# Performance work log

Hardware: AMD Instinct MI355X
Metric: run time of the kernel (lower is better)

## Reference

```python
import jax, jax.numpy as jnp
import numpy as np

C_CLAMP = 0.5
EPSILON = 1e-6
L_START = 0

BATCH, SEQ, D_MODEL, N_EXPERTS, RANK = 4, 8192, 1024, 16, 16


def setup_inputs() -> dict:
    key = jax.random.key(0)
    k_x, k_w, k_a, k_b, k_s = jax.random.split(key, 5)
    x = jax.random.normal(k_x, (BATCH, SEQ, D_MODEL), dtype=jnp.float32)
    # base nn.Linear params
    W = jax.random.normal(k_w, (D_MODEL, D_MODEL), dtype=jnp.float32) * 0.02
    b = jnp.zeros((D_MODEL,), dtype=jnp.float32)
    # stacked per-expert LoRA factors: A_e [in, r], B_e [r, out]
    A = jax.random.normal(k_a, (N_EXPERTS, D_MODEL, RANK), dtype=jnp.float32) * 0.02
    B_mat = jax.random.normal(k_b, (N_EXPERTS, RANK, D_MODEL), dtype=jnp.float32) * 0.02
    # routing scores p_score per active expert
    scores = jax.random.uniform(k_s, (N_EXPERTS,), dtype=jnp.float32)
    layer_idx = 5  # static python int, >= L_START so adapters are injected
    return {"x": x, "W": W, "b": b, "A": A, "B_mat": B_mat,
            "scores": scores, "layer_idx": layer_idx}


def reference(x, W, b, A, B_mat, scores, layer_idx):
    # base linear: z = x @ W^T + b
    z = jnp.einsum('bsd,Dd->bsD', x, W) + b
    if layer_idx is not None and layer_idx < L_START:
        return z
    # m = sum_e p_e * (x @ A_e @ B_e), batched low-rank adapter sum
    xa = jnp.einsum('bsd,edr->ebsr', x, A)          # [E, B, S, r]
    m = jnp.einsum('e,ebsr,erD->bsD', scores, xa, B_mat)
    # norm-ratio clamp epilogue
    norm_z = jnp.linalg.norm(z, axis=-1, keepdims=True)
    norm_m = jnp.linalg.norm(m, axis=-1, keepdims=True)
    gamma = jnp.minimum(C_CLAMP * norm_z / (norm_m + EPSILON), 1.0)
    return z + gamma * m
```

## Files before the change

kernel.cpp:

```cpp
#include <hip/hip_runtime.h>

typedef __attribute__((ext_vector_type(8))) __bf16 bf16x8;
typedef __attribute__((ext_vector_type(8))) unsigned short u16x8;
typedef __attribute__((ext_vector_type(4))) float f32x4;

__device__ inline unsigned short f2bf(float f) {
    union { float f; unsigned int i; } v; v.f = f;
    unsigned int i = v.i;
    unsigned int r = i + 0x7FFFu + ((i >> 16) & 1u);
    return (unsigned short)(r >> 16);
}
__device__ inline float bf2f(unsigned short u) {
    union { unsigned int i; float f; } v; v.i = ((unsigned int)u) << 16; return v.f;
}

__device__ inline void gload_lds16(const void* g, void* l) {
    __builtin_amdgcn_global_load_lds(
        (const __attribute__((address_space(1))) unsigned int*)g,
        (__attribute__((address_space(3))) unsigned int*)l, 16, 0, 0);
}

__device__ inline bf16x8 ldsrd(unsigned off) {
    bf16x8 r;
    asm volatile("ds_read_b128 %0, %1" : "=v"(r) : "v"(off));
    return r;
}

__global__ __launch_bounds__(256) void cast_x(const float* __restrict__ x,
                                              unsigned short* __restrict__ xb, int n4) {
    int idx = blockIdx.x * blockDim.x + threadIdx.x;
    int stride = gridDim.x * blockDim.x;
    for (int i = idx; i < n4; i += stride) {
        float4 v = ((const float4*)x)[i];
        ushort4 o;
        o.x = f2bf(v.x); o.y = f2bf(v.y); o.z = f2bf(v.z); o.w = f2bf(v.w);
        ((ushort4*)xb)[i] = o;
    }
}

__global__ __launch_bounds__(256) void cast_w(const float* __restrict__ W,
                                              unsigned short* __restrict__ wcat) {
    int i = blockIdx.x * 256 + threadIdx.x;
    float4 v = ((const float4*)W)[i];
    ushort4 o;
    o.x = f2bf(v.x); o.y = f2bf(v.y); o.z = f2bf(v.z); o.w = f2bf(v.w);
    ((ushort4*)wcat)[i] = o;
}

__global__ __launch_bounds__(256) void prep_acat(const float* __restrict__ A,
                                                 const float* __restrict__ scores,
                                                 unsigned short* __restrict__ acat) {
    int tid = blockIdx.x * 256 + threadIdx.x;
    int e = tid >> 10;
    int d = tid & 1023;
    float pe = scores[e];
    const float4* src = (const float4*)(A + (size_t)e * 16384 + (size_t)d * 16);
    unsigned short* dst = acat + (size_t)d * 256 + e * 16;
    #pragma unroll
    for (int q = 0; q < 4; ++q) {
        float4 v = src[q];
        ushort4 o;
        o.x = f2bf(pe * v.x); o.y = f2bf(pe * v.y);
        o.z = f2bf(pe * v.z); o.w = f2bf(pe * v.w);
        *(ushort4*)(dst + q * 4) = o;
    }
}

__global__ __launch_bounds__(256) void prep_bcat(const float* __restrict__ Bm,
                                                 unsigned short* __restrict__ bcatT) {
    __shared__ float t[64][65];
    const int tx = threadIdx.x;
    const int Dt = (blockIdx.x & 15) * 64;
    const int et = (blockIdx.x >> 4) * 64;
    {
        const int i = tx >> 2;
        const int c4 = (tx & 3) * 16;
        const float* src = Bm + (size_t)(et + i) * 1024 + Dt + c4;
        #pragma unroll
        for (int q = 0; q < 4; ++q) {
            float4 v = *(const float4*)(src + q * 4);
            t[i][c4 + q * 4 + 0] = v.x; t[i][c4 + q * 4 + 1] = v.y;
            t[i][c4 + q * 4 + 2] = v.z; t[i][c4 + q * 4 + 3] = v.w;
        }
    }
    __syncthreads();
    {
        const int j = tx >> 2;
        const int seg = (tx & 3) * 16;
        unsigned short* dst = bcatT + (size_t)(Dt + j) * 256 + et + seg;
        #pragma unroll
        for (int q = 0; q < 16; ++q)
            dst[q] = f2bf(t[seg + q][j]);
    }
}

__global__ __launch_bounds__(256) void mini_gemm(const unsigned short* __restrict__ bcatT,
                                                 const unsigned short* __restrict__ acat,
                                                 unsigned short* __restrict__ wcat) {
    extern __shared__ char lds[];
    const int tid = threadIdx.x;
    const int l = tid & 63;
    const int w = tid >> 6;
    const int wr = w >> 1;
    const int wc = w & 1;

    const int trow = (blockIdx.x >> 3) * 128;
    const int tcol = (blockIdx.x & 7) * 128;

    const unsigned rA128 = (unsigned)((wr * 64 + (l & 15)) * 128);
    const unsigned rB128 = 16384u + (unsigned)((wc * 64 + (l & 15)) * 128);
    const unsigned pck0 = (((l >> 4)) ^ (l & 7)) * 16u;
    const unsigned pck1 = ((4 + (l >> 4)) ^ (l & 7)) * 16u;

    const unsigned strow = (unsigned)(tid >> 3);
    const unsigned stchunk = (unsigned)((tid & 7) ^ (strow & 7));
    const unsigned stlds = (unsigned)(tid * 16);

    f32x4 acc[4][4] = {};

    for (int t = 0; t < 4; ++t) {
        #pragma unroll
        for (int h = 0; h < 4; ++h) {
            const unsigned short* ga = bcatT + (size_t)(trow + h * 32 + strow) * 256 + t * 64 + stchunk * 8;
            const unsigned short* gb = acat  + (size_t)(tcol + h * 32 + strow) * 256 + t * 64 + stchunk * 8;
            gload_lds16(ga, lds + h * 4096 + stlds);
            gload_lds16(gb, lds + 16384 + h * 4096 + stlds);
        }
        asm volatile("s_waitcnt vmcnt(0)" ::: "memory");
        __builtin_amdgcn_s_barrier();

        bf16x8 a[4], b[4];
        #pragma unroll
        for (int ks = 0; ks < 2; ++ks) {
            const unsigned pck = ks ? pck1 : pck0;
            #pragma unroll
            for (int mf = 0; mf < 4; ++mf) a[mf] = ldsrd(rA128 + mf * 2048 + pck);
            #pragma unroll
            for (int nf = 0; nf < 4; ++nf) b[nf] = ldsrd(rB128 + nf * 2048 + pck);
            asm volatile("s_waitcnt lgkmcnt(0)" ::: "memory");
            __builtin_amdgcn_sched_barrier(0);
            #pragma unroll
            for (int mf = 0; mf < 4; ++mf)
                #pragma unroll
                for (int nf = 0; nf < 4; ++nf)
                    acc[mf][nf] = __builtin_amdgcn_mfma_f32_16x16x32_bf16(a[mf], b[nf], acc[mf][nf], 0, 0, 0);
        }
        __builtin_amdgcn_s_barrier();
    }

    const int crow0 = trow + wr * 64 + (l >> 4) * 4;
    const int ccol0 = tcol + wc * 64 + (l & 15);
    #pragma unroll
    for (int mf = 0; mf < 4; ++mf) {
        int D = crow0 + mf * 16;
        #pragma unroll
        for (int nf = 0; nf < 4; ++nf) {
            int d = ccol0 + nf * 16;
            f32x4 v = acc[mf][nf];
            #pragma unroll
            for (int j = 0; j < 4; ++j)
                wcat[(size_t)(1024 + D + j) * 1024 + d] = f2bf(v[j]);
        }
    }
}

__global__ __launch_bounds__(512, 2) void gemm_zm4(const unsigned short* __restrict__ xb,
                                                   const unsigned short* __restrict__ wcat,
                                                   const float* __restrict__ bias,
                                                   float* __restrict__ zout) {
    extern __shared__ char lds[];
    const int tid = threadIdx.x;
    const int l = tid & 63;
    const int w = tid >> 6;
    const int wr = w >> 2;
    const int wc = w & 3;

    const int bid = blockIdx.x;
    const int swz = (bid & 7) * 128 + (bid >> 3);
    const int brow = (swz >> 3) * 256;
    const int bcol = (swz & 7) * 256;

    const unsigned rA128 = (unsigned)((wr * 64 + (l & 15)) * 128);
    const unsigned rB128 = 32768u + (unsigned)((wc * 64 + (l & 15)) * 128);
    const unsigned pck0 = (((l >> 4)) ^ (l & 7)) * 16u;
    const unsigned pck1 = ((4 + (l >> 4)) ^ (l & 7)) * 16u;

    const unsigned strow = (unsigned)(tid >> 3);
    const unsigned stchunk = (unsigned)((tid & 7) ^ (strow & 7));
    const unsigned stlds = (unsigned)(tid * 16);

    f32x4 acc[8][4] = {};

#define STAGE(mat, baserow, T, h, bofs) do {                                        \
        int T_ = (T); int Ts_ = T_ > 15 ? 15 : T_;                                  \
        unsigned db_ = (unsigned)((T_ & 1) * 65536) + (bofs) + (h) * 16384u;        \
        const unsigned short* g_ = (mat) + (size_t)((baserow) + (h) * 128 + strow) * 1024 \
                                   + Ts_ * 64 + stchunk * 8;                        \
        gload_lds16(g_,           lds + db_ + stlds);                               \
        gload_lds16(g_ + 64*1024, lds + db_ + 8192 + stlds);                        \
    } while (0)

#define LGKM0_SB() do {                                                             \
        asm volatile("s_waitcnt lgkmcnt(0)" ::: "memory");                          \
        __builtin_amdgcn_sched_barrier(0);                                          \
    } while (0)

#define VMCNT_SB(N) do {                                                            \
        asm volatile("s_waitcnt vmcnt(" #N ")" ::: "memory");                       \
        __builtin_amdgcn_sched_barrier(0);                                          \
    } while (0)

#define RD_A4(dst, bufo, MBASE, PCK) do {                                           \
        dst[0] = ldsrd((bufo) + rA128 + ((MBASE + 0) & 3) * 2048 + ((MBASE + 0) >> 2) * 16384 + (PCK)); \
        dst[1] = ldsrd((bufo) + rA128 + ((MBASE + 1) & 3) * 2048 + ((MBASE + 1) >> 2) * 16384 + (PCK)); \
        dst[2] = ldsrd((bufo) + rA128 + ((MBASE + 2) & 3) * 2048 + ((MBASE + 2) >> 2) * 16384 + (PCK)); \
        dst[3] = ldsrd((bufo) + rA128 + ((MBASE + 3) & 3) * 2048 + ((MBASE + 3) >> 2) * 16384 + (PCK)); \
    } while (0)

#define RD_B4(dst, bufo, PCK) do {                                                  \
        dst[0] = ldsrd((bufo) + rB128 + 0 * 2048 + (PCK));                          \
        dst[1] = ldsrd((bufo) + rB128 + 1 * 2048 + (PCK));                          \
        dst[2] = ldsrd((bufo) + rB128 + 2 * 2048 + (PCK));                          \
        dst[3] = ldsrd((bufo) + rB128 + 3 * 2048 + (PCK));                          \
    } while (0)

#define MFMA16(ABASE, AFR, BFR) do {                                                \
        __builtin_amdgcn_s_setprio(1);                                              \
        _Pragma("unroll")                                                           \
        for (int nf = 0; nf < 4; ++nf) {                                            \
            acc[ABASE + 0][nf] = __builtin_amdgcn_mfma_f32_16x16x32_bf16(AFR[0], BFR[nf], acc[ABASE + 0][nf], 0, 0, 0); \
            acc[ABASE + 1][nf] = __builtin_amdgcn_mfma_f32_16x16x32_bf16(AFR[1], BFR[nf], acc[ABASE + 1][nf], 0, 0, 0); \
            acc[ABASE + 2][nf] = __builtin_amdgcn_mfma_f32_16x16x32_bf16(AFR[2], BFR[nf], acc[ABASE + 2][nf], 0, 0, 0); \
            acc[ABASE + 3][nf] = __builtin_amdgcn_mfma_f32_16x16x32_bf16(AFR[3], BFR[nf], acc[ABASE + 3][nf], 0, 0, 0); \
        }                                                                           \
        __builtin_amdgcn_s_setprio(0);                                              \
    } while (0)

    STAGE(xb,   brow, 0, 0, 0u);
    STAGE(wcat, bcol, 0, 0, 32768u);
    STAGE(wcat, bcol, 0, 1, 32768u);
    STAGE(xb,   brow, 0, 1, 0u);
    VMCNT_SB(2);
    __builtin_amdgcn_s_barrier();

    for (int t = 0; t < 16; ++t) {
        const unsigned bufo = (unsigned)((t & 1) * 65536);
        bf16x8 aL[4], aL2[4], aH[4], aH2[4], b0[4], b1[4];

        RD_A4(aL, bufo, 0, pck0);
        RD_B4(b0, bufo, pck0);
        STAGE(xb, brow, t + 1, 0, 0u);
        __builtin_amdgcn_s_barrier();
        LGKM0_SB();
        MFMA16(0, aL, b0);

        RD_A4(aL2, bufo, 0, pck1);
        RD_B4(b1, bufo, pck1);
        STAGE(wcat, bcol, t + 1, 0, 32768u);
        VMCNT_SB(4);
        __builtin_amdgcn_s_barrier();
        LGKM0_SB();
        MFMA16(0, aL2, b1);

        RD_A4(aH, bufo, 4, pck0);
        STAGE(wcat, bcol, t + 1, 1, 32768u);
        __builtin_amdgcn_s_barrier();
        LGKM0_SB();
        MFMA16(4, aH, b0);

        RD_A4(aH2, bufo, 4, pck1);
        STAGE(xb, brow, t + 1, 1, 0u);
        VMCNT_SB(2);
        __builtin_amdgcn_s_barrier();
        LGKM0_SB();
        MFMA16(4, aH2, b1);
    }

    asm volatile("s_waitcnt vmcnt(0)" ::: "memory");
    __builtin_amdgcn_s_barrier();

    unsigned short* tlds = (unsigned short*)lds;
    const bool is_z = (bcol < 1024);
    {
        const int crow = wr * 64 + (l >> 4) * 4;
        const int ccol = wc * 64 + (l & 15);
        #pragma unroll
        for (int nf = 0; nf < 4; ++nf) {
            int col = ccol + nf * 16;
            float bb = is_z ? bias[bcol + col] : 0.f;
            #pragma unroll
            for (int mf = 0; mf < 8; ++mf) {
                int row = crow + (mf & 3) * 16 + (mf >> 2) * 128;
                f32x4 v = acc[mf][nf];
                #pragma unroll
                for (int j = 0; j < 4; ++j)
                    tlds[(row + j) * 256 + col] = f2bf(v[j] + bb);
            }
        }
    }
    __syncthreads();
    {
        unsigned short* og = (unsigned short*)zout;
        const int rr = tid >> 5;
        const int c16 = (tid & 31) * 8;
        #pragma unroll
        for (int p = 0; p < 16; ++p) {
            int row = p * 16 + rr;
            u16x8 v = *(const u16x8*)&tlds[row * 256 + c16];
            *(u16x8*)&og[(size_t)(brow + row) * 2048 + bcol + c16] = v;
        }
    }
#undef STAGE
#undef LGKM0_SB
#undef VMCNT_SB
#undef RD_A4
#undef RD_B4
#undef MFMA16
}

__global__ __launch_bounds__(256) void epilogue_ip(float* out, const int* __restrict__ lidx) {
    int row = blockIdx.x;
    int tx = threadIdx.x;
    const unsigned short* io = (const unsigned short*)out;
    size_t base = (size_t)row * 2048;

    ushort4 zv = *(const ushort4*)&io[base + tx * 4];
    ushort4 mv = *(const ushort4*)&io[base + 1024 + tx * 4];
    float z0 = bf2f(zv.x), z1 = bf2f(zv.y), z2 = bf2f(zv.z), z3 = bf2f(zv.w);
    float m0 = bf2f(mv.x), m1 = bf2f(mv.y), m2 = bf2f(mv.z), m3 = bf2f(mv.w);

    float sz = z0 * z0 + z1 * z1 + z2 * z2 + z3 * z3;
    float sm = m0 * m0 + m1 * m1 + m2 * m2 + m3 * m3;

    #pragma unroll
    for (int off = 32; off > 0; off >>= 1) {
        sz += __shfl_xor(sz, off);
        sm += __shfl_xor(sm, off);
    }
    __shared__ float red[8];
    int wv = tx >> 6;
    if ((tx & 63) == 0) { red[wv * 2] = sz; red[wv * 2 + 1] = sm; }
    __syncthreads();
    sz = red[0] + red[2] + red[4] + red[6];
    sm = red[1] + red[3] + red[5] + red[7];

    float gamma = fminf(0.5f * sqrtf(sz) / (sqrtf(sm) + 1e-6f), 1.0f);
    if (lidx[0] < 0) gamma = 0.f;

    float4 o;
    o.x = z0 + gamma * m0; o.y = z1 + gamma * m1;
    o.z = z2 + gamma * m2; o.w = z3 + gamma * m3;
    *(float4*)&out[(size_t)row * 1024 + tx * 4] = o;
}

extern "C" void kernel_launch(void* const* d_in, const int* in_sizes, int n_in,
                              void* d_out, int out_size, void* d_ws, size_t ws_size,
                              hipStream_t stream) {
    const float* x  = (const float*)d_in[0];
    const float* W  = (const float*)d_in[1];
    const float* b  = (const float*)d_in[2];
    const float* A  = (const float*)d_in[3];
    const float* Bm = (const float*)d_in[4];
    const float* sc = (const float*)d_in[5];
    const int* lidx = (const int*)d_in[6];
    float* out = (float*)d_out;

    unsigned short* xb    = (unsigned short*)d_ws;
    unsigned short* wcat  = (unsigned short*)((char*)d_ws + 67108864);
    unsigned short* acat  = (unsigned short*)((char*)d_ws + 71303168);
    unsigned short* bcatT = (unsigned short*)((char*)d_ws + 71827456);

    hipFuncSetAttribute((const void*)gemm_zm4,
                        hipFuncAttributeMaxDynamicSharedMemorySize, 131072);

    cast_x<<<2048, 256, 0, stream>>>(x, xb, 33554432 / 4);
    cast_w<<<1024, 256, 0, stream>>>(W, wcat);
    prep_acat<<<64, 256, 0, stream>>>(A, sc, acat);
    prep_bcat<<<64, 256, 0, stream>>>(Bm, bcatT);
    mini_gemm<<<64, 256, 32768, stream>>>(bcatT, acat, wcat);
    gemm_zm4<<<1024, 512, 131072, stream>>>(xb, wcat, b, out);
    epilogue_ip<<<32768, 256, 0, stream>>>(out, lidx);
}
```

Measured before the change: 221.5 us.

## Halve GEMM K-tile to 32 to cut LDS to 64KB for two blocks per CU

The main GEMM's K-step shrinks from 64 to 32, so each double-buffered stage uses half the LDS (64KB total instead of 128KB). This should let two 512-thread blocks share a CU. The pipeline is rebuilt around two MFMA phases per iteration with 32 iterations and a new 4-chunk XOR swizzle. The epilogue now stages output through LDS in two 128-row halves so it fits the smaller buffer. In exchange there are twice as many barriers and waitcnt syncs per unit of work, and less MFMA work is issued between them.

```diff
diff --git a/kernel.cpp b/kernel.cpp
--- a/kernel.cpp
+++ b/kernel.cpp
@@ -164,10 +164,10 @@
     }
 }
 
-__global__ __launch_bounds__(512, 2) void gemm_zm4(const unsigned short* __restrict__ xb,
-                                                   const unsigned short* __restrict__ wcat,
-                                                   const float* __restrict__ bias,
-                                                   float* __restrict__ zout) {
+__global__ __launch_bounds__(512, 2) void gemm_2b(const unsigned short* __restrict__ xb,
+                                                  const unsigned short* __restrict__ wcat,
+                                                  const float* __restrict__ bias,
+                                                  float* __restrict__ zout) {
     extern __shared__ char lds[];
     const int tid = threadIdx.x;
     const int l = tid & 63;
@@ -180,24 +180,22 @@
     const int brow = (swz >> 3) * 256;
     const int bcol = (swz & 7) * 256;
 
-    const unsigned rA128 = (unsigned)((wr * 64 + (l & 15)) * 128);
-    const unsigned rB128 = 32768u + (unsigned)((wc * 64 + (l & 15)) * 128);
-    const unsigned pck0 = (((l >> 4)) ^ (l & 7)) * 16u;
-    const unsigned pck1 = ((4 + (l >> 4)) ^ (l & 7)) * 16u;
-
-    const unsigned strow = (unsigned)(tid >> 3);
-    const unsigned stchunk = (unsigned)((tid & 7) ^ (strow & 7));
+    const unsigned rA = (unsigned)((wr * 64 + (l & 15)) * 64);
+    const unsigned rB = 16384u + (unsigned)((wc * 64 + (l & 15)) * 64);
+    const unsigned pck = (unsigned)(((l >> 4) ^ (l & 3)) * 16);
+
+    const unsigned srow = (unsigned)(tid >> 2);
+    const unsigned schunk = (unsigned)((tid & 3) ^ (srow & 3));
     const unsigned stlds = (unsigned)(tid * 16);
 
     f32x4 acc[8][4] = {};
 
-#define STAGE(mat, baserow, T, h, bofs) do {                                        \
-        int T_ = (T); int Ts_ = T_ > 15 ? 15 : T_;                                  \
-        unsigned db_ = (unsigned)((T_ & 1) * 65536) + (bofs) + (h) * 16384u;        \
-        const unsigned short* g_ = (mat) + (size_t)((baserow) + (h) * 128 + strow) * 1024 \
-                                   + Ts_ * 64 + stchunk * 8;                        \
-        gload_lds16(g_,           lds + db_ + stlds);                               \
-        gload_lds16(g_ + 64*1024, lds + db_ + 8192 + stlds);                        \
+#define STAGE_U(mat, baserow, T, h, matofs) do {                                    \
+        int T_ = (T); int Ts_ = T_ > 31 ? 31 : T_;                                  \
+        unsigned db_ = (unsigned)((T_ & 1) * 32768) + (matofs) + (h) * 8192u;       \
+        const unsigned short* g_ = (mat) + (size_t)((baserow) + (h) * 128 + srow) * 1024 \
+                                   + Ts_ * 32 + schunk * 8;                         \
+        gload_lds16(g_, lds + db_ + stlds);                                         \
     } while (0)
 
 #define LGKM0_SB() do {                                                             \
@@ -210,18 +208,18 @@
         __builtin_amdgcn_sched_barrier(0);                                          \
     } while (0)
 
-#define RD_A4(dst, bufo, MBASE, PCK) do {                                           \
-        dst[0] = ldsrd((bufo) + rA128 + ((MBASE + 0) & 3) * 2048 + ((MBASE + 0) >> 2) * 16384 + (PCK)); \
-        dst[1] = ldsrd((bufo) + rA128 + ((MBASE + 1) & 3) * 2048 + ((MBASE + 1) >> 2) * 16384 + (PCK)); \
-        dst[2] = ldsrd((bufo) + rA128 + ((MBASE + 2) & 3) * 2048 + ((MBASE + 2) >> 2) * 16384 + (PCK)); \
-        dst[3] = ldsrd((bufo) + rA128 + ((MBASE + 3) & 3) * 2048 + ((MBASE + 3) >> 2) * 16384 + (PCK)); \
-    } while (0)
-
-#define RD_B4(dst, bufo, PCK) do {                                                  \
-        dst[0] = ldsrd((bufo) + rB128 + 0 * 2048 + (PCK));                          \
-        dst[1] = ldsrd((bufo) + rB128 + 1 * 2048 + (PCK));                          \
-        dst[2] = ldsrd((bufo) + rB128 + 2 * 2048 + (PCK));                          \
-        dst[3] = ldsrd((bufo) + rB128 + 3 * 2048 + (PCK));                          \
+#define RD_A4(dst, bufo, MBASE) do {                                                \
+        dst[0] = ldsrd((bufo) + rA + ((MBASE) >> 2) * 8192 + 0 * 1024 + pck);       \
+        dst[1] = ldsrd((bufo) + rA + ((MBASE) >> 2) * 8192 + 1 * 1024 + pck);       \
+        dst[2] = ldsrd((bufo) + rA + ((MBASE) >> 2) * 8192 + 2 * 1024 + pck);       \
+        dst[3] = ldsrd((bufo) + rA + ((MBASE) >> 2) * 8192 + 3 * 1024 + pck);       \
+    } while (0)
+
+#define RD_B4(dst, bufo) do {                                                       \
+        dst[0] = ldsrd((bufo) + rB + 0 * 1024 + pck);                               \
+        dst[1] = ldsrd((bufo) + rB + 1 * 1024 + pck);                               \
+        dst[2] = ldsrd((bufo) + rB + 2 * 1024 + pck);                               \
+        dst[3] = ldsrd((bufo) + rB + 3 * 1024 + pck);                               \
     } while (0)
 
 #define MFMA16(ABASE, AFR, BFR) do {                                                \
@@ -236,81 +234,74 @@
         __builtin_amdgcn_s_setprio(0);                                              \
     } while (0)
 
-    STAGE(xb,   brow, 0, 0, 0u);
-    STAGE(wcat, bcol, 0, 0, 32768u);
-    STAGE(wcat, bcol, 0, 1, 32768u);
-    STAGE(xb,   brow, 0, 1, 0u);
-    VMCNT_SB(2);
+    STAGE_U(xb,   brow, 0, 0, 0u);
+    STAGE_U(wcat, bcol, 0, 0, 16384u);
+    STAGE_U(wcat, bcol, 0, 1, 16384u);
+    STAGE_U(xb,   brow, 0, 1, 0u);
+    VMCNT_SB(0);
     __builtin_amdgcn_s_barrier();
 
-    for (int t = 0; t < 16; ++t) {
-        const unsigned bufo = (unsigned)((t & 1) * 65536);
-        bf16x8 aL[4], aL2[4], aH[4], aH2[4], b0[4], b1[4];
-
-        RD_A4(aL, bufo, 0, pck0);
-        RD_B4(b0, bufo, pck0);
-        STAGE(xb, brow, t + 1, 0, 0u);
+    for (int t = 0; t < 32; ++t) {
+        const unsigned bufo = (unsigned)((t & 1) * 32768);
+        bf16x8 aL[4], aH[4], b[4];
+
+        RD_A4(aL, bufo, 0);
+        RD_B4(b, bufo);
+        STAGE_U(xb,   brow, t + 1, 0, 0u);
+        STAGE_U(wcat, bcol, t + 1, 0, 16384u);
+        STAGE_U(wcat, bcol, t + 1, 1, 16384u);
+        VMCNT_SB(3);
         __builtin_amdgcn_s_barrier();
         LGKM0_SB();
-        MFMA16(0, aL, b0);
-
-        RD_A4(aL2, bufo, 0, pck1);
-        RD_B4(b1, bufo, pck1);
-        STAGE(wcat, bcol, t + 1, 0, 32768u);
-        VMCNT_SB(4);
+        MFMA16(0, aL, b);
+
+        RD_A4(aH, bufo, 4);
+        STAGE_U(xb, brow, t + 1, 1, 0u);
+        VMCNT_SB(1);
         __builtin_amdgcn_s_barrier();
         LGKM0_SB();
-        MFMA16(0, aL2, b1);
-
-        RD_A4(aH, bufo, 4, pck0);
-        STAGE(wcat, bcol, t + 1, 1, 32768u);
-        __builtin_amdgcn_s_barrier();
-        LGKM0_SB();
-        MFMA16(4, aH, b0);
-
-        RD_A4(aH2, bufo, 4, pck1);
-        STAGE(xb, brow, t + 1, 1, 0u);
-        VMCNT_SB(2);
-        __builtin_amdgcn_s_barrier();
-        LGKM0_SB();
-        MFMA16(4, aH2, b1);
+        MFMA16(4, aH, b);
     }
 
     asm volatile("s_waitcnt vmcnt(0)" ::: "memory");
     __builtin_amdgcn_s_barrier();
 
     unsigned short* tlds = (unsigned short*)lds;
+    unsigned short* og = (unsigned short*)zout;
     const bool is_z = (bcol < 1024);
-    {
-        const int crow = wr * 64 + (l >> 4) * 4;
-        const int ccol = wc * 64 + (l & 15);
-        #pragma unroll
-        for (int nf = 0; nf < 4; ++nf) {
-            int col = ccol + nf * 16;
-            float bb = is_z ? bias[bcol + col] : 0.f;
-            #pragma unroll
-            for (int mf = 0; mf < 8; ++mf) {
-                int row = crow + (mf & 3) * 16 + (mf >> 2) * 128;
-                f32x4 v = acc[mf][nf];
+    #pragma unroll
+    for (int half = 0; half < 2; ++half) {
+        {
+            const int crow = wr * 64 + (l >> 4) * 4;
+            const int ccol = wc * 64 + (l & 15);
+            #pragma unroll
+            for (int nf = 0; nf < 4; ++nf) {
+                int col = ccol + nf * 16;
+                float bb = is_z ? bias[bcol + col] : 0.f;
                 #pragma unroll
-                for (int j = 0; j < 4; ++j)
-                    tlds[(row + j) * 256 + col] = f2bf(v[j] + bb);
+                for (int m4 = 0; m4 < 4; ++m4) {
+                    int row = crow + m4 * 16;
+                    f32x4 v = acc[half * 4 + m4][nf];
+                    #pragma unroll
+                    for (int j = 0; j < 4; ++j)
+                        tlds[(row + j) * 256 + col] = f2bf(v[j] + bb);
+                }
             }
         }
-    }
-    __syncthreads();
-    {
-        unsigned short* og = (unsigned short*)zout;
-        const int rr = tid >> 5;
-        const int c16 = (tid & 31) * 8;
-        #pragma unroll
-        for (int p = 0; p < 16; ++p) {
-            int row = p * 16 + rr;
-            u16x8 v = *(const u16x8*)&tlds[row * 256 + c16];
-            *(u16x8*)&og[(size_t)(brow + row) * 2048 + bcol + c16] = v;
-        }
-    }
-#undef STAGE
+        __syncthreads();
+        {
+            const int rr = tid >> 5;
+            const int c16 = (tid & 31) * 8;
+            #pragma unroll
+            for (int p = 0; p < 8; ++p) {
+                int row = p * 16 + rr;
+                u16x8 v = *(const u16x8*)&tlds[row * 256 + c16];
+                *(u16x8*)&og[(size_t)(brow + half * 128 + row) * 2048 + bcol + c16] = v;
+            }
+        }
+        __syncthreads();
+    }
+#undef STAGE_U
 #undef LGKM0_SB
 #undef VMCNT_SB
 #undef RD_A4
@@ -370,14 +361,14 @@
     unsigned short* acat  = (unsigned short*)((char*)d_ws + 71303168);
     unsigned short* bcatT = (unsigned short*)((char*)d_ws + 71827456);
 
-    hipFuncSetAttribute((const void*)gemm_zm4,
-                        hipFuncAttributeMaxDynamicSharedMemorySize, 131072);
+    hipFuncSetAttribute((const void*)gemm_2b,
+                        hipFuncAttributeMaxDynamicSharedMemorySize, 65536);
 
     cast_x<<<2048, 256, 0, stream>>>(x, xb, 33554432 / 4);
     cast_w<<<1024, 256, 0, stream>>>(W, wcat);
     prep_acat<<<64, 256, 0, stream>>>(A, sc, acat);
     prep_bcat<<<64, 256, 0, stream>>>(Bm, bcatT);
     mini_gemm<<<64, 256, 32768, stream>>>(bcatT, acat, wcat);
-    gemm_zm4<<<1024, 512, 131072, stream>>>(xb, wcat, b, out);
+    gemm_2b<<<1024, 512, 65536, stream>>>(xb, wcat, b, out);
     epilogue_ip<<<32768, 256, 0, stream>>>(out, lidx);
 }
```

Result: slower. 239.2 us (+7.9%).
